# Kernel optimization log

Hardware: AMD Instinct MI355X
Metric: run time of the kernel (lower is better)

## Reference

```python
import jax, jax.numpy as jnp
import numpy as np

HEADS = 16
DIM_HEAD = 64
LN_EPS = 1e-5


def setup_inputs() -> dict:
    key = jax.random.key(0)
    ks = jax.random.split(key, 4)
    b, n, dim = 2, 2048, 1024
    inner = HEADS * DIM_HEAD
    x = jax.random.normal(ks[0], (b, n, dim), dtype=jnp.float32)
    gamma = jnp.ones((dim,), dtype=jnp.float32)
    beta = jnp.zeros((dim,), dtype=jnp.float32)
    w_qkv = jax.random.normal(ks[1], (dim, 3 * inner), dtype=jnp.float32) * (dim ** -0.5)
    w_out = jax.random.normal(ks[2], (inner, dim), dtype=jnp.float32) * (inner ** -0.5)
    b_out = jnp.zeros((dim,), dtype=jnp.float32)
    return {"x": x, "gamma": gamma, "beta": beta, "w_qkv": w_qkv, "w_out": w_out, "b_out": b_out}


def reference(x, gamma, beta, w_qkv, w_out, b_out):
    b, n, dim = x.shape
    h, d = HEADS, DIM_HEAD
    scale = d ** -0.5
    # LayerNorm
    mu = jnp.mean(x, axis=-1, keepdims=True)
    var = jnp.mean(jnp.square(x - mu), axis=-1, keepdims=True)
    xn = (x - mu) * jax.lax.rsqrt(var + LN_EPS) * gamma + beta
    # QKV projection (no bias)
    qkv = xn @ w_qkv  # [b, n, 3*h*d]
    q, k, v = jnp.split(qkv, 3, axis=-1)
    split_heads = lambda t: t.reshape(b, n, h, d).transpose(0, 2, 1, 3)  # [b, h, n, d]
    q, k, v = split_heads(q), split_heads(k), split_heads(v)
    q = q * scale
    sim = jnp.einsum('bhid,bhjd->bhij', q, k)  # full O(n^2) score matrix
    attn = jax.nn.softmax(sim, axis=-1)
    out = jnp.einsum('bhij,bhjd->bhid', attn, v)
    out = out.transpose(0, 2, 1, 3).reshape(b, n, h * d)
    return out @ w_out + b_out
```

## Files before the change

kernel.cpp:

```cpp
#include <hip/hip_runtime.h>
#include <hip/hip_bf16.h>

#define HEADS 16
#define DH 64
#define DIM 1024
#define SEQ 2048
#define BATCH 2
#define ROWS (BATCH*SEQ)
#define NQKV (3*DIM)
#define NKVT (SEQ/64)
#define NSPLIT 3
#define QSCALE 0.18033688011112042f
#define NBH (BATCH*HEADS)
#define NQROWS (NBH*SEQ)

typedef __attribute__((ext_vector_type(8))) short bf16x8;
typedef __attribute__((ext_vector_type(4))) float f32x4;
typedef __attribute__((ext_vector_type(16))) float f32x16;
typedef __attribute__((ext_vector_type(4))) unsigned u32x4;
typedef __hip_bfloat16 bf16;

static __device__ __forceinline__ bf16 f2bf(float v){ return __float2bfloat16(v); }

static __device__ __forceinline__ unsigned cvtpk(float a, float b){
  unsigned r;
  asm("v_cvt_pk_bf16_f32 %0, %1, %2" : "=v"(r) : "v"(a), "v"(b));
  return r;
}

static __device__ __forceinline__ void gload16(const void* g, void* lds){
  __builtin_amdgcn_global_load_lds((const __attribute__((address_space(1))) void*)g,
                                   (__attribute__((address_space(3))) void*)lds, 16, 0, 0);
}

__global__ __launch_bounds__(256) void prep_kernel(
    const float* __restrict__ x, const float* __restrict__ gamma,
    const float* __restrict__ beta, bf16* __restrict__ xn,
    const float* __restrict__ w_qkv, bf16* __restrict__ wqt,
    const float* __restrict__ w_out, bf16* __restrict__ wot)
{
  __shared__ float red[8];
  __shared__ __align__(16) bf16 tt[64][72];
  int bid = blockIdx.x;
  int tid = threadIdx.x;
  if (bid < ROWS){
    int row = bid;
    float4 v = ((const float4*)(x + (size_t)row*DIM))[tid];
    float s  = v.x+v.y+v.z+v.w;
    float ss = v.x*v.x+v.y*v.y+v.z*v.z+v.w*v.w;
    #pragma unroll
    for (int m=1;m<64;m<<=1){ s += __shfl_xor(s,m); ss += __shfl_xor(ss,m); }
    int wid = tid>>6;
    if ((tid&63)==0){ red[wid]=s; red[4+wid]=ss; }
    __syncthreads();
    s  = red[0]+red[1]+red[2]+red[3];
    ss = red[4]+red[5]+red[6]+red[7];
    float mu  = s*(1.0f/DIM);
    float var = ss*(1.0f/DIM) - mu*mu;
    float inv = rsqrtf(var + 1e-5f);
    float4 g  = ((const float4*)gamma)[tid];
    float4 bb = ((const float4*)beta)[tid];
    __align__(8) bf16 o[4];
    o[0]=f2bf((v.x-mu)*inv*g.x+bb.x);
    o[1]=f2bf((v.y-mu)*inv*g.y+bb.y);
    o[2]=f2bf((v.z-mu)*inv*g.z+bb.z);
    o[3]=f2bf((v.w-mu)*inv*g.w+bb.w);
    *(uint2*)&xn[(size_t)row*DIM + tid*4] = *(const uint2*)o;
    return;
  }
  const float* in; bf16* out; int R, C, bx, by;
  if (bid < ROWS + 768){
    int idx = bid - ROWS; bx = idx % 48; by = idx / 48;
    in = w_qkv; out = wqt; R = DIM; C = NQKV;
  } else {
    int idx = bid - ROWS - 768; bx = idx % 16; by = idx / 16;
    in = w_out; out = wot; R = DIM; C = DIM;
  }
  int c0 = bx*64, r0 = by*64;
  int row = tid>>2;
  int cq  = (tid&3)*16;
  #pragma unroll
  for (int j=0;j<4;j++){
    float4 v = *(const float4*)&in[(size_t)(r0+row)*C + c0 + cq + j*4];
    tt[cq+j*4+0][row] = f2bf(v.x);
    tt[cq+j*4+1][row] = f2bf(v.y);
    tt[cq+j*4+2][row] = f2bf(v.z);
    tt[cq+j*4+3][row] = f2bf(v.w);
  }
  __syncthreads();
  int c = tid>>2; int rq = (tid&3)*16;
  uint4 u0 = *(const uint4*)&tt[c][rq];
  uint4 u1 = *(const uint4*)&tt[c][rq+8];
  *(uint4*)&out[(size_t)(c0+c)*R + r0 + rq]     = u0;
  *(uint4*)&out[(size_t)(c0+c)*R + r0 + rq + 8] = u1;
}

template<int BM>
__global__ __launch_bounds__(256) void gemm_bt(
    const bf16* __restrict__ A, const bf16* __restrict__ Bt, int K, int mode,
    bf16* __restrict__ qb, bf16* __restrict__ kb, bf16* __restrict__ vtb,
    float* __restrict__ outf, const float* __restrict__ bias)
{
  constexpr int MT = (BM == 128) ? 4 : 2;
  __shared__ __align__(16) bf16 aL[3][BM*32];
  __shared__ __align__(16) bf16 bL[3][128*32];
  int tid = threadIdx.x;
  int w = tid>>6, l = tid&63;
  int lr = l&15, lh = l>>4;
  int wr = w>>1, wc = w&1;
  int by = blockIdx.y, bx = blockIdx.x;
  const bf16* Ab = A  + (size_t)(by*BM)*K;
  const bf16* Bb = Bt + (size_t)(bx*128)*K;
  int srow = w*32 + (l>>2);
  int scol = ((l&3)*8) ^ (((l>>2)&3)<<3);
  int frsw = (lr&3)<<3;
  int nt = K/32;

  f32x4 acc[MT][4] = {};

  auto STAGE = [&](int buf, int k0){
    if constexpr (BM == 128){
      gload16(Ab + (size_t)(srow   )*K + k0 + scol, &aL[buf][w*1024      ]);
      gload16(Ab + (size_t)(srow+16)*K + k0 + scol, &aL[buf][w*1024 + 512]);
    } else {
      gload16(Ab + (size_t)(tid>>2 )*K + k0 + scol, &aL[buf][w*512       ]);
    }
    gload16(Bb + (size_t)(srow   )*K + k0 + scol, &bL[buf][w*1024      ]);
    gload16(Bb + (size_t)(srow+16)*K + k0 + scol, &bL[buf][w*1024 + 512]);
  };

  auto COMPUTE = [&](int buf){
    bf16x8 af[MT], bfr[4];
    #pragma unroll
    for (int m=0;m<MT;m++)
      af[m]  = *(const bf16x8*)&aL[buf][(wr*(MT*16) + m*16 + lr)*32 + ((lh*8) ^ frsw)];
    #pragma unroll
    for (int n=0;n<4;n++)
      bfr[n] = *(const bf16x8*)&bL[buf][(wc*64 + n*16 + lr)*32 + ((lh*8) ^ frsw)];
    #pragma unroll
    for (int m=0;m<MT;m++)
      #pragma unroll
      for (int n=0;n<4;n++)
        acc[m][n] = __builtin_amdgcn_mfma_f32_16x16x32_bf16(af[m], bfr[n], acc[m][n], 0,0,0);
  };

  STAGE(0, 0);
  STAGE(1, 32);
  int cur = 0;
  for (int t=0; t<nt-1; t++){
    if constexpr (BM == 128) asm volatile("s_waitcnt vmcnt(4)" ::: "memory");
    else                     asm volatile("s_waitcnt vmcnt(3)" ::: "memory");
    __builtin_amdgcn_s_barrier();
    __builtin_amdgcn_sched_barrier(0);
    int s2 = cur + 2; if (s2 >= 3) s2 -= 3;
    if (t+2 < nt) STAGE(s2, (t+2)*32);
    COMPUTE(cur);
    cur = (cur == 2) ? 0 : cur + 1;
  }
  asm volatile("s_waitcnt vmcnt(0)" ::: "memory");
  __builtin_amdgcn_s_barrier();
  __builtin_amdgcn_sched_barrier(0);
  COMPUTE(cur);

  int rb = by*BM + wr*(MT*16), cb = bx*128 + wc*64;
  if (mode == 1){
    #pragma unroll
    for (int m=0;m<MT;m++)
      #pragma unroll
      for (int n=0;n<4;n++)
        #pragma unroll
        for (int reg=0;reg<4;reg++){
          int r = rb + m*16 + lh*4 + reg;
          int c = cb + n*16 + lr;
          outf[(size_t)r*DIM + c] = acc[m][n][reg] + bias[c];
        }
  } else if (bx < 8){
    int b = rb >> 11;
    int nn0 = rb & 2047;
    #pragma unroll
    for (int m=0;m<MT;m++)
      #pragma unroll
      for (int n=0;n<4;n++)
        #pragma unroll
        for (int reg=0;reg<4;reg++){
          int nn = nn0 + m*16 + lh*4 + reg;
          int c  = cb + n*16 + lr;
          int hh = c >> 6, dd = c & 63;
          qb[((size_t)(b*HEADS + hh)*SEQ + nn)*DH + dd] = f2bf(acc[m][n][reg]*QSCALE);
        }
  } else if (bx < 16){
    int b = rb >> 11;
    int kvt = (rb & 2047) >> 6;
    int hh0 = ((cb - 1024) >> 6);
    #pragma unroll
    for (int m=0;m<MT;m++)
      #pragma unroll
      for (int reg=0;reg<4;reg++){
        int kvi = m*16 + lh*4 + reg;
        int sw  = (kvi&7)<<3;
        #pragma unroll
        for (int n=0;n<4;n++){
          int dd = n*16 + lr;
          kb[((size_t)(b*HEADS + hh0)*NKVT + kvt)*4096 + kvi*64 + (dd ^ sw)] = f2bf(acc[m][n][reg]);
        }
      }
  } else {
    __syncthreads();
    bf16* tl = (w < 2 ? (bf16*)aL : (bf16*)bL) + (w&1)*4096;
    int b   = rb >> 11;
    int kvt = (rb & 2047) >> 6;
    int hh  = (cb - 2048) >> 6;
    #pragma unroll
    for (int n=0;n<4;n++){
      int dd = n*16 + lr;
      int sw = (dd&7)<<3;
      #pragma unroll
      for (int m=0;m<MT;m++)
        #pragma unroll
        for (int reg=0;reg<4;reg++)
          tl[dd*64 + ((m*16 + lh*4 + reg) ^ sw)] = f2bf(acc[m][n][reg]);
    }
    __syncthreads();
    size_t gb = ((size_t)(b*HEADS + hh)*NKVT + kvt)*4096;
    #pragma unroll
    for (int j=0;j<8;j++)
      *(uint4*)&vtb[gb + j*512 + l*8] = *(const uint4*)&tl[j*512 + l*8];
  }
}

__global__ __launch_bounds__(256,4) void attn_part(
    const bf16* __restrict__ qb, const bf16* __restrict__ kb,
    const bf16* __restrict__ vtb,
    bf16* __restrict__ Opart, float* __restrict__ Mpart, float* __restrict__ Spart)
{
  __shared__ __align__(16) bf16 Kl[2][4096];
  __shared__ __align__(16) bf16 Vl[4096];
  int tid = threadIdx.x;
  int w = tid>>6, l = tid&63;
  int q5 = l & 31;
  int hi = l >> 5;
  int swz = (q5&7)<<3;
  int bh = blockIdx.y;
  int sp = blockIdx.z;
  int ts = sp*11, te = (sp==2) ? 32 : ts+11;
  const bf16* Q  = qb  + (size_t)bh*SEQ*DH;
  const bf16* Kt = kb  + (size_t)bh*NKVT*4096;
  const bf16* Vt = vtb + (size_t)bh*NKVT*4096;
  int q0w = blockIdx.x*128 + w*32;

  int co[4];
  #pragma unroll
  for (int st=0;st<4;st++) co[st] = (st*16 + hi*8) ^ swz;
  int r0 = q5*64, r1 = r0 + 2048;

  bf16x8 qf[4];
  #pragma unroll
  for (int st=0;st<4;st++)
    qf[st] = *(const bf16x8*)&Q[(size_t)(q0w + q5)*DH + st*16 + hi*8];

  bf16x8 vone;
  #pragma unroll
  for (int i=0;i<8;i++) vone[i] = (short)0x3f80;

  f32x16 o0 = {}, o1 = {}, osum = {};
  float mrun = -3e38f;

  gload16(Kt + (size_t)ts*4096 + w*1024       + l*8, &Kl[0][w*1024      ]);
  gload16(Kt + (size_t)ts*4096 + w*1024 + 512 + l*8, &Kl[0][w*1024 + 512]);

  for (int t=ts; t<te; t++){
    int cur = (t-ts)&1;
    __syncthreads();
    gload16(Vt + (size_t)t*4096 + w*1024       + l*8, &Vl[w*1024      ]);
    gload16(Vt + (size_t)t*4096 + w*1024 + 512 + l*8, &Vl[w*1024 + 512]);
    bool havek = (t+1 < te);
    if (havek){
      gload16(Kt + (size_t)(t+1)*4096 + w*1024       + l*8, &Kl[cur^1][w*1024      ]);
      gload16(Kt + (size_t)(t+1)*4096 + w*1024 + 512 + l*8, &Kl[cur^1][w*1024 + 512]);
    }
    f32x16 s0 = {}, s1 = {};
    __builtin_amdgcn_s_setprio(1);
    #pragma unroll
    for (int st=0;st<4;st++){
      bf16x8 kf0 = *(const bf16x8*)&Kl[cur][r0 + co[st]];
      bf16x8 kf1 = *(const bf16x8*)&Kl[cur][r1 + co[st]];
      s0 = __builtin_amdgcn_mfma_f32_32x32x16_bf16(kf0, qf[st], s0, 0,0,0);
      s1 = __builtin_amdgcn_mfma_f32_32x32x16_bf16(kf1, qf[st], s1, 0,0,0);
    }
    __builtin_amdgcn_s_setprio(0);
    float pm = -3e38f;
    #pragma unroll
    for (int r=0;r<16;r++) pm = fmaxf(fmaxf(pm, s0[r]), s1[r]);
    pm = fmaxf(pm, __shfl_xor(pm, 32));
    if (__any(pm > mrun + 8.f)){
      float mn = fmaxf(mrun, pm);
      float sc = __builtin_amdgcn_exp2f(mrun - mn);
      mrun = mn;
      #pragma unroll
      for (int reg=0;reg<16;reg++){
        float scr = __shfl(sc, (l & 32) | ((reg&3) + 8*(reg>>2) + 4*hi));
        o0[reg] *= scr;
        o1[reg] *= scr;
        osum[reg] *= scr;
      }
    }
    #pragma unroll
    for (int r=0;r<16;r++){
      s0[r] = __builtin_amdgcn_exp2f(s0[r] - mrun);
      s1[r] = __builtin_amdgcn_exp2f(s1[r] - mrun);
    }
    if (havek) asm volatile("s_waitcnt vmcnt(2)" ::: "memory");
    else       asm volatile("s_waitcnt vmcnt(0)" ::: "memory");
    __builtin_amdgcn_s_barrier();
    __builtin_amdgcn_sched_barrier(0);
    #define PV_STEP(SV, SGN, KVS)                                                    \
    {                                                                                \
      unsigned Aw = cvtpk(SV[SGN+0], SV[SGN+1]);                                     \
      unsigned Bw = cvtpk(SV[SGN+2], SV[SGN+3]);                                     \
      unsigned Cw = cvtpk(SV[SGN+4], SV[SGN+5]);                                     \
      unsigned Dw = cvtpk(SV[SGN+6], SV[SGN+7]);                                     \
      asm volatile("v_permlane32_swap_b32 %0, %1" : "+v"(Aw), "+v"(Cw));             \
      asm volatile("v_permlane32_swap_b32 %0, %1" : "+v"(Bw), "+v"(Dw));             \
      u32x4 pw = {Aw, Bw, Cw, Dw};                                                   \
      bf16x8 pa = *(const bf16x8*)&pw;                                               \
      bf16x8 vf0 = *(const bf16x8*)&Vl[r0 + co[KVS]];                                \
      bf16x8 vf1 = *(const bf16x8*)&Vl[r1 + co[KVS]];                                \
      __builtin_amdgcn_s_setprio(1);                                                 \
      o0 = __builtin_amdgcn_mfma_f32_32x32x16_bf16(pa, vf0, o0, 0,0,0);              \
      o1 = __builtin_amdgcn_mfma_f32_32x32x16_bf16(pa, vf1, o1, 0,0,0);              \
      osum = __builtin_amdgcn_mfma_f32_32x32x16_bf16(pa, vone, osum, 0,0,0);         \
      __builtin_amdgcn_s_setprio(0);                                                 \
    }
    PV_STEP(s0, 0, 0)
    PV_STEP(s0, 8, 1)
    PV_STEP(s1, 0, 2)
    PV_STEP(s1, 8, 3)
    #undef PV_STEP
  }
  size_t rbase = ((size_t)sp*NBH + bh)*SEQ;
  #pragma unroll
  for (int reg=0;reg<16;reg++){
    int q = q0w + (reg&3) + 8*(reg>>2) + 4*hi;
    Opart[(rbase + q)*64 + q5]      = f2bf(o0[reg]);
    Opart[(rbase + q)*64 + 32 + q5] = f2bf(o1[reg]);
  }
  if (l < 32)
    Mpart[rbase + q0w + l] = mrun;
  if (q5 == 0){
    #pragma unroll
    for (int reg=0;reg<16;reg++){
      int q = q0w + (reg&3) + 8*(reg>>2) + 4*hi;
      Spart[rbase + q] = osum[reg];
    }
  }
}

__global__ __launch_bounds__(256) void attn_merge(
    const bf16* __restrict__ Opart, const float* __restrict__ Mpart,
    const float* __restrict__ Spart, bf16* __restrict__ ao)
{
  int r = blockIdx.x*4 + (threadIdx.x>>6);
  int d = threadIdx.x & 63;
  float m0 = Mpart[r], m1 = Mpart[NQROWS + r], m2 = Mpart[2*NQROWS + r];
  float m  = fmaxf(fmaxf(m0, m1), m2);
  float c0 = exp2f(m0 - m), c1 = exp2f(m1 - m), c2 = exp2f(m2 - m);
  float denom = Spart[r]*c0 + Spart[NQROWS + r]*c1 + Spart[2*NQROWS + r]*c2;
  float v = __bfloat162float(Opart[(size_t)r*64 + d])*c0
          + __bfloat162float(Opart[((size_t)NQROWS + r)*64 + d])*c1
          + __bfloat162float(Opart[((size_t)2*NQROWS + r)*64 + d])*c2;
  int bh = r >> 11, q = r & 2047;
  int b = bh >> 4, h = bh & 15;
  ao[((size_t)(b*SEQ + q))*DIM + h*DH + d] = f2bf(v / denom);
}

extern "C" void kernel_launch(void* const* d_in, const int* in_sizes, int n_in,
                              void* d_out, int out_size, void* d_ws, size_t ws_size,
                              hipStream_t stream)
{
  const float* x     = (const float*)d_in[0];
  const float* gamma = (const float*)d_in[1];
  const float* beta  = (const float*)d_in[2];
  const float* w_qkv = (const float*)d_in[3];
  const float* w_out = (const float*)d_in[4];
  const float* b_out = (const float*)d_in[5];
  float* out = (float*)d_out;

  bf16* ws  = (bf16*)d_ws;
  bf16* xn  = ws;
  bf16* wqt = xn  + (size_t)ROWS*DIM;
  bf16* wot = wqt + (size_t)NQKV*DIM;
  bf16* qb  = wot + (size_t)DIM*DIM;
  bf16* kb  = qb  + (size_t)NBH*SEQ*DH;
  bf16* vtb = kb  + (size_t)NBH*SEQ*DH;
  bf16* ao  = vtb + (size_t)NBH*SEQ*DH;
  bf16* Opart = ao + (size_t)ROWS*DIM;
  float* Mpart = (float*)(Opart + (size_t)NSPLIT*NQROWS*DH);
  float* Spart = Mpart + (size_t)NSPLIT*NQROWS;

  prep_kernel<<<dim3(ROWS + 768 + 256), dim3(256), 0, stream>>>(
      x, gamma, beta, xn, w_qkv, wqt, w_out, wot);
  gemm_bt<128><<<dim3(NQKV/128, ROWS/128), dim3(256), 0, stream>>>(
      xn, wqt, DIM, 0, qb, kb, vtb, (float*)nullptr, (const float*)nullptr);
  attn_part<<<dim3(SEQ/128, NBH, NSPLIT), dim3(256), 0, stream>>>(
      qb, kb, vtb, Opart, Mpart, Spart);
  attn_merge<<<dim3(NQROWS/4), dim3(256), 0, stream>>>(Opart, Mpart, Spart, ao);
  gemm_bt<64><<<dim3(DIM/128, ROWS/64), dim3(256), 0, stream>>>(
      ao, wot, DIM, 1, (bf16*)nullptr, (bf16*)nullptr, (bf16*)nullptr, out, b_out);
}
```

Measured before the change: 135.9 us.

## Double-buffer V tiles and reduce KV split count to two

The attention kernel now gives V its own double buffer in LDS and prefetches both K and V for the next tile at the top of each iteration. This lets it drop the mid-iteration vmcnt wait and extra barrier that used to stall on the V load. The KV sequence split drops from three to two, so each block handles 16 tiles and the merge kernel combines only two partials. The grid becomes 1024 blocks, which should fit in a single wave at the declared occupancy instead of leaving a partial second wave. The costs are less parallelism per query tile and more LDS per block.

Measured after the change: 124.3 us. -8.6%, faster.

```diff
diff --git a/kernel.cpp b/kernel.cpp
--- a/kernel.cpp
+++ b/kernel.cpp
@@ -9,7 +9,7 @@
 #define ROWS (BATCH*SEQ)
 #define NQKV (3*DIM)
 #define NKVT (SEQ/64)
-#define NSPLIT 3
+#define NSPLIT 2
 #define QSCALE 0.18033688011112042f
 #define NBH (BATCH*HEADS)
 #define NQROWS (NBH*SEQ)
@@ -234,7 +234,7 @@
     bf16* __restrict__ Opart, float* __restrict__ Mpart, float* __restrict__ Spart)
 {
   __shared__ __align__(16) bf16 Kl[2][4096];
-  __shared__ __align__(16) bf16 Vl[4096];
+  __shared__ __align__(16) bf16 Vl[2][4096];
   int tid = threadIdx.x;
   int w = tid>>6, l = tid&63;
   int q5 = l & 31;
@@ -242,7 +242,7 @@
   int swz = (q5&7)<<3;
   int bh = blockIdx.y;
   int sp = blockIdx.z;
-  int ts = sp*11, te = (sp==2) ? 32 : ts+11;
+  int ts = sp*16, te = ts+16;
   const bf16* Q  = qb  + (size_t)bh*SEQ*DH;
   const bf16* Kt = kb  + (size_t)bh*NKVT*4096;
   const bf16* Vt = vtb + (size_t)bh*NKVT*4096;
@@ -265,18 +265,25 @@
   f32x16 o0 = {}, o1 = {}, osum = {};
   float mrun = -3e38f;
 
-  gload16(Kt + (size_t)ts*4096 + w*1024       + l*8, &Kl[0][w*1024      ]);
-  gload16(Kt + (size_t)ts*4096 + w*1024 + 512 + l*8, &Kl[0][w*1024 + 512]);
+  {
+    const bf16* ks = Kt + (size_t)ts*4096;
+    const bf16* vs = Vt + (size_t)ts*4096;
+    gload16(ks + w*1024       + l*8, &Kl[0][w*1024      ]);
+    gload16(ks + w*1024 + 512 + l*8, &Kl[0][w*1024 + 512]);
+    gload16(vs + w*1024       + l*8, &Vl[0][w*1024      ]);
+    gload16(vs + w*1024 + 512 + l*8, &Vl[0][w*1024 + 512]);
+  }
 
   for (int t=ts; t<te; t++){
     int cur = (t-ts)&1;
     __syncthreads();
-    gload16(Vt + (size_t)t*4096 + w*1024       + l*8, &Vl[w*1024      ]);
-    gload16(Vt + (size_t)t*4096 + w*1024 + 512 + l*8, &Vl[w*1024 + 512]);
-    bool havek = (t+1 < te);
-    if (havek){
-      gload16(Kt + (size_t)(t+1)*4096 + w*1024       + l*8, &Kl[cur^1][w*1024      ]);
-      gload16(Kt + (size_t)(t+1)*4096 + w*1024 + 512 + l*8, &Kl[cur^1][w*1024 + 512]);
+    if (t+1 < te){
+      const bf16* ks = Kt + (size_t)(t+1)*4096;
+      const bf16* vs = Vt + (size_t)(t+1)*4096;
+      gload16(ks + w*1024       + l*8, &Kl[cur^1][w*1024      ]);
+      gload16(ks + w*1024 + 512 + l*8, &Kl[cur^1][w*1024 + 512]);
+      gload16(vs + w*1024       + l*8, &Vl[cur^1][w*1024      ]);
+      gload16(vs + w*1024 + 512 + l*8, &Vl[cur^1][w*1024 + 512]);
     }
     f32x16 s0 = {}, s1 = {};
     __builtin_amdgcn_s_setprio(1);
@@ -309,10 +316,6 @@
       s0[r] = __builtin_amdgcn_exp2f(s0[r] - mrun);
       s1[r] = __builtin_amdgcn_exp2f(s1[r] - mrun);
     }
-    if (havek) asm volatile("s_waitcnt vmcnt(2)" ::: "memory");
-    else       asm volatile("s_waitcnt vmcnt(0)" ::: "memory");
-    __builtin_amdgcn_s_barrier();
-    __builtin_amdgcn_sched_barrier(0);
     #define PV_STEP(SV, SGN, KVS)                                                    \
     {                                                                                \
       unsigned Aw = cvtpk(SV[SGN+0], SV[SGN+1]);                                     \
@@ -323,8 +326,8 @@
       asm volatile("v_permlane32_swap_b32 %0, %1" : "+v"(Bw), "+v"(Dw));             \
       u32x4 pw = {Aw, Bw, Cw, Dw};                                                   \
       bf16x8 pa = *(const bf16x8*)&pw;                                               \
-      bf16x8 vf0 = *(const bf16x8*)&Vl[r0 + co[KVS]];                                \
-      bf16x8 vf1 = *(const bf16x8*)&Vl[r1 + co[KVS]];                                \
+      bf16x8 vf0 = *(const bf16x8*)&Vl[cur][r0 + co[KVS]];                           \
+      bf16x8 vf1 = *(const bf16x8*)&Vl[cur][r1 + co[KVS]];                           \
       __builtin_amdgcn_s_setprio(1);                                                 \
       o0 = __builtin_amdgcn_mfma_f32_32x32x16_bf16(pa, vf0, o0, 0,0,0);              \
       o1 = __builtin_amdgcn_mfma_f32_32x32x16_bf16(pa, vf1, o1, 0,0,0);              \
@@ -361,13 +364,12 @@
 {
   int r = blockIdx.x*4 + (threadIdx.x>>6);
   int d = threadIdx.x & 63;
-  float m0 = Mpart[r], m1 = Mpart[NQROWS + r], m2 = Mpart[2*NQROWS + r];
-  float m  = fmaxf(fmaxf(m0, m1), m2);
-  float c0 = exp2f(m0 - m), c1 = exp2f(m1 - m), c2 = exp2f(m2 - m);
-  float denom = Spart[r]*c0 + Spart[NQROWS + r]*c1 + Spart[2*NQROWS + r]*c2;
+  float m0 = Mpart[r], m1 = Mpart[NQROWS + r];
+  float m  = fmaxf(m0, m1);
+  float c0 = exp2f(m0 - m), c1 = exp2f(m1 - m);
+  float denom = Spart[r]*c0 + Spart[NQROWS + r]*c1;
   float v = __bfloat162float(Opart[(size_t)r*64 + d])*c0
-          + __bfloat162float(Opart[((size_t)NQROWS + r)*64 + d])*c1
-          + __bfloat162float(Opart[((size_t)2*NQROWS + r)*64 + d])*c2;
+          + __bfloat162float(Opart[((size_t)NQROWS + r)*64 + d])*c1;
   int bh = r >> 11, q = r & 2047;
   int b = bh >> 4, h = bh & 15;
   ao[((size_t)(b*SEQ + q))*DIM + h*DH + d] = f2bf(v / denom);
```
